# Kernel tuning notes

Hardware: AMD Instinct MI355X
Metric: run time of the kernel (lower is better)

## Reference

```python
import jax, jax.numpy as jnp
import numpy as np

DIM = 2048
H = 16
DK = 128
DV = 128
KCONV = 4
EPS = 1e-6
B = 2
S = 2048
KD = H * DK  # 2048
VD = H * DV  # 2048


def setup_inputs() -> dict:
    key = jax.random.key(0)
    ks = jax.random.split(key, 16)
    sc = 0.02
    inp = {
        "x": jax.random.normal(ks[0], (B, S, DIM), dtype=jnp.float32),
        "Wq": jax.random.normal(ks[1], (KD, DIM), dtype=jnp.float32) * sc,
        "Wk": jax.random.normal(ks[2], (KD, DIM), dtype=jnp.float32) * sc,
        "Wv": jax.random.normal(ks[3], (VD, DIM), dtype=jnp.float32) * sc,
        "Wa": jax.random.normal(ks[4], (H, DIM), dtype=jnp.float32) * sc,
        "Wb": jax.random.normal(ks[5], (H, DIM), dtype=jnp.float32) * sc,
        "Wg": jax.random.normal(ks[6], (VD, DIM), dtype=jnp.float32) * sc,
        "Wo": jax.random.normal(ks[7], (DIM, VD), dtype=jnp.float32) * sc,
        "cw_q": jax.random.normal(ks[8], (KD, KCONV), dtype=jnp.float32) * 0.3,
        "cb_q": jnp.zeros((KD,), dtype=jnp.float32),
        "cw_k": jax.random.normal(ks[9], (KD, KCONV), dtype=jnp.float32) * 0.3,
        "cb_k": jnp.zeros((KD,), dtype=jnp.float32),
        "cw_v": jax.random.normal(ks[10], (VD, KCONV), dtype=jnp.float32) * 0.3,
        "cb_v": jnp.zeros((VD,), dtype=jnp.float32),
        "A_log": jnp.zeros((H,), dtype=jnp.float32),
        "dt_bias": jnp.zeros((H,), dtype=jnp.float32),
        "norm_w": jnp.ones((VD,), dtype=jnp.float32),
    }
    return inp


def _causal_conv(x, w, b):
    # x: [B, S, C]; w: [C, K]; b: [C]. Depthwise causal conv (zero init state) + SiLU.
    Bb, Ss, C = x.shape
    xp = jnp.pad(x, ((0, 0), (KCONV - 1, 0), (0, 0)))
    out = b
    for j in range(KCONV):
        out = out + xp[:, j:j + Ss, :] * w[:, j]
    return jax.nn.silu(out)


def _l2norm(x):
    n = jnp.sqrt(jnp.sum(x * x, axis=-1, keepdims=True))
    return x / jnp.maximum(n, 1e-12)


def _forward(x, Wq, Wk, Wv, Wa, Wb, Wg, Wo, cw_q, cb_q, cw_k, cb_k, cw_v, cb_v,
             A_log, dt_bias, norm_w):
    Bb, Ss, _ = x.shape
    q = _causal_conv(x @ Wq.T, cw_q, cb_q)  # [B,S,KD]
    k = _causal_conv(x @ Wk.T, cw_k, cb_k)
    v = _causal_conv(x @ Wv.T, cw_v, cb_v)

    a = x @ Wa.T  # [B,S,H]
    b = x @ Wb.T
    g = jnp.exp(-jnp.exp(A_log)[None, None, :] * jax.nn.softplus(a + dt_bias[None, None, :]))
    beta = jax.nn.sigmoid(b)

    q = _l2norm(q.reshape(Bb, Ss, H, DK))
    k = _l2norm(k.reshape(Bb, Ss, H, DK))
    v = v.reshape(Bb, Ss, H, DV)

    S0 = jnp.zeros((Bb, H, DK, DV), dtype=x.dtype)

    def step(Sstate, inputs):
        q_t, k_t, v_t, g_t, beta_t = inputs  # [B,H,DK],[B,H,DK],[B,H,DV],[B,H],[B,H]
        retrieved = jnp.einsum('bhkv,bhk->bhv', Sstate, k_t)
        error = v_t - g_t[..., None] * retrieved
        update = k_t[..., :, None] * (beta_t[..., None] * error)[..., None, :]
        Snew = g_t[..., None, None] * Sstate + update
        o_t = jnp.einsum('bhkv,bhk->bhv', Snew, q_t)
        return Snew, o_t

    # scan over time: move time axis to front
    xs = (q.transpose(1, 0, 2, 3), k.transpose(1, 0, 2, 3), v.transpose(1, 0, 2, 3),
          g.transpose(1, 0, 2), beta.transpose(1, 0, 2))
    _, o = jax.lax.scan(step, S0, xs)  # o: [S,B,H,DV]
    o = o.transpose(1, 0, 2, 3).reshape(Bb, Ss, VD)

    # RMSNorm
    o = o * jax.lax.rsqrt(jnp.mean(o * o, axis=-1, keepdims=True) + EPS) * norm_w
    o = o * jax.nn.silu(x @ Wg.T)
    return o @ Wo.T


def reference(x, Wq, Wk, Wv, Wa, Wb, Wg, Wo, cw_q, cb_q, cw_k, cb_k, cw_v, cb_v,
              A_log, dt_bias, norm_w):
    return _forward(x, Wq, Wk, Wv, Wa, Wb, Wg, Wo, cw_q, cb_q, cw_k, cb_k,
                    cw_v, cb_v, A_log, dt_bias, norm_w)
```

## Files before the change

### kernel.cpp

```cpp
#include <hip/hip_runtime.h>

#define S_LEN   2048
#define NH      16
#define DIM     2048
#define KD      2048
#define VD      2048
#define MB      1048576ull
#define CT      64
#define NC      32

typedef short  short8  __attribute__((ext_vector_type(8)));
typedef short  short4v __attribute__((ext_vector_type(4)));
typedef float  floatx4 __attribute__((ext_vector_type(4)));

#define MFMA(a, b, c) __builtin_amdgcn_mfma_f32_16x16x32_bf16((a), (b), (c), 0, 0, 0)

__device__ inline short f2bf(float x) {
    unsigned u = __float_as_uint(x);
    unsigned r = (u + 0x7fffu + ((u >> 16) & 1u)) >> 16;
    return (short)r;
}
__device__ inline float bf2f(short s) {
    return __uint_as_float(((unsigned)(unsigned short)s) << 16);
}
__device__ inline float silu_f(float x) { return x / (1.f + __expf(-x)); }

__device__ inline short8 neg8(short8 a) {
    unsigned* p = (unsigned*)&a;
    p[0] ^= 0x80008000u; p[1] ^= 0x80008000u;
    p[2] ^= 0x80008000u; p[3] ^= 0x80008000u;
    return a;
}

__device__ inline void load_lds16(const void* g, void* l) {
    __builtin_amdgcn_global_load_lds(
        (const __attribute__((address_space(1))) unsigned int*)g,
        (__attribute__((address_space(3))) unsigned int*)l, 16, 0, 0);
}

__device__ inline void store_c(float* C, size_t idx, float v) { C[idx] = v; }
__device__ inline void store_c(short* C, size_t idx, float v) { C[idx] = f2bf(v); }

__device__ __forceinline__ void lds_barrier() {
    asm volatile("s_waitcnt lgkmcnt(0)" ::: "memory");
    __builtin_amdgcn_s_barrier();
}

__global__ __launch_bounds__(256) void cvt_all_kernel(
    const float* __restrict__ x,  const float* __restrict__ Wq,
    const float* __restrict__ Wk, const float* __restrict__ Wv,
    const float* __restrict__ Wg, const float* __restrict__ Wo,
    short* __restrict__ xb,  short* __restrict__ Wqb, short* __restrict__ Wkb,
    short* __restrict__ Wvb, short* __restrict__ Wgb, short* __restrict__ Wob) {
    const float* in; short* out; int n8;
    switch (blockIdx.y) {
        case 0:  in = x;  out = xb;  n8 = 1048576; break;
        case 1:  in = Wq; out = Wqb; n8 = 524288;  break;
        case 2:  in = Wk; out = Wkb; n8 = 524288;  break;
        case 3:  in = Wv; out = Wvb; n8 = 524288;  break;
        case 4:  in = Wg; out = Wgb; n8 = 524288;  break;
        default: in = Wo; out = Wob; n8 = 524288;  break;
    }
    int i = blockIdx.x * 256 + threadIdx.x;
    if (i >= n8) return;
    float4 a = ((const float4*)in)[2 * i];
    float4 b = ((const float4*)in)[2 * i + 1];
    short8 o;
    o[0] = f2bf(a.x); o[1] = f2bf(a.y); o[2] = f2bf(a.z); o[3] = f2bf(a.w);
    o[4] = f2bf(b.x); o[5] = f2bf(b.y); o[6] = f2bf(b.z); o[7] = f2bf(b.w);
    ((short8*)out)[i] = o;
}


#define VM(n_) asm volatile("s_waitcnt vmcnt(" #n_ ")" ::: "memory");

#define STAGE8(s_, isB_)                                                     \
    {                                                                        \
        const char* gsrc = (isB_) ? (const char*)Bw : (const char*)A;        \
        int t0 = (isB_) ? n0 : m0;                                           \
        char* dbase = smem + ((s_) & 3) * 32768 + (isB_) * 16384;            \
        _Pragma("unroll")                                                    \
        for (int ld = 0; ld < 2; ++ld) {                                     \
            int ch = ld * 8 + wave;                                          \
            int Pl = (ch << 10) + (lane << 4);                               \
            int Q  = Pl ^ (((lane >> 3) & 3) << 4);                          \
            const char* src = gsrc + ((size_t)(t0 + (Q >> 6)) << 12)         \
                              + ((size_t)(s_) << 6) + (Q & 63);              \
            load_lds16(src, dbase + (ch << 10));                             \
        }                                                                    \
    }

#define PHASE8(s_, qm_, LOADB_, STG, WAIT)                                   \
    {                                                                        \
        const char* sb = smem + ((s_) & 3) * 32768;                          \
        short8 af[4];                                                        \
        if (LOADB_) {                                                        \
            _Pragma("unroll")                                                \
            for (int nf = 0; nf < 4; ++nf)                                   \
                bfr[nf] = *(const short8*)(sb + 16384 +                      \
                    ((rowB_base + nf * 16) << 6) + qsw);                     \
        }                                                                    \
        _Pragma("unroll")                                                    \
        for (int mf = 0; mf < 4; ++mf)                                       \
            af[mf] = *(const short8*)(sb +                                   \
                ((rowA_base + (qm_) * 64 + mf * 16) << 6) + qsw);            \
        STG                                                                  \
        __builtin_amdgcn_s_barrier();                                        \
        asm volatile("s_waitcnt lgkmcnt(0)" ::: "memory");                   \
        __builtin_amdgcn_s_setprio(1);                                       \
        _Pragma("unroll")                                                    \
        for (int mf = 0; mf < 4; ++mf)                                       \
            _Pragma("unroll")                                                \
            for (int nf = 0; nf < 4; ++nf)                                   \
                acc[(qm_) * 4 + mf][nf] =                                    \
                    MFMA(af[mf], bfr[nf], acc[(qm_) * 4 + mf][nf]);          \
        __builtin_amdgcn_s_setprio(0);                                       \
        WAIT                                                                 \
        __builtin_amdgcn_s_barrier();                                        \
    }

template <typename OutT>
__device__ __forceinline__ void gemm8_tile(const short* __restrict__ A,
                                           const short* __restrict__ Bw,
                                           OutT* __restrict__ C, char* smem) {
    int x  = blockIdx.x;
    int xs = (x & 7) * 16 + (x >> 3);
    int m0 = (xs >> 3) * 256;
    int n0 = (xs & 7) * 256;
    int tid  = threadIdx.x;
    int wave = tid >> 6, lane = tid & 63;
    int l16  = lane & 15, quad = lane >> 4;
    int wm = wave >> 2, wn = wave & 3;
    int qsw = ((quad ^ ((l16 >> 1) & 3)) << 4);
    int rowA_base = wm * 128 + l16;
    int rowB_base = wn * 64 + l16;

    floatx4 acc[8][4];
#pragma unroll
    for (int i = 0; i < 8; ++i)
#pragma unroll
        for (int j = 0; j < 4; ++j) acc[i][j] = (floatx4){0.f, 0.f, 0.f, 0.f};
    short8 bfr[4];

    STAGE8(0, 0) STAGE8(0, 1)
    STAGE8(1, 0) STAGE8(1, 1)
    STAGE8(2, 0) STAGE8(2, 1)
    VM(8)
    __builtin_amdgcn_s_barrier();

#pragma unroll 1
    for (int T = 0; T < 30; ++T) {
        int s0 = 2 * T, s1 = 2 * T + 1, sa = 2 * T + 3, sb2 = 2 * T + 4;
        PHASE8(s0, 0, 1, STAGE8(sa, 0), )
        PHASE8(s0, 1, 0, STAGE8(sa, 1), VM(8))
        PHASE8(s1, 0, 1, STAGE8(sb2, 0), )
        PHASE8(s1, 1, 0, STAGE8(sb2, 1), VM(8))
    }
    PHASE8(60, 0, 1, STAGE8(63, 0), )
    PHASE8(60, 1, 0, STAGE8(63, 1), VM(8))
    PHASE8(61, 0, 1, , )
    PHASE8(61, 1, 0, , VM(4))
    PHASE8(62, 0, 1, , )
    PHASE8(62, 1, 0, , VM(0))
    PHASE8(63, 0, 1, , )
    PHASE8(63, 1, 0, , )

#pragma unroll
    for (int i = 0; i < 8; ++i) {
        int row0 = m0 + wm * 128 + (i >> 2) * 64 + (i & 3) * 16 + quad * 4;
#pragma unroll
        for (int nf = 0; nf < 4; ++nf) {
            int col = n0 + wn * 64 + nf * 16 + l16;
#pragma unroll
            for (int r = 0; r < 4; ++r)
                store_c(C, (size_t)(row0 + r) * 2048 + col, acc[i][nf][r]);
        }
    }
}

__global__ __launch_bounds__(512) void gemm8_qkvg(const short* __restrict__ A,
    const short* __restrict__ B0, const short* __restrict__ B1,
    const short* __restrict__ B2, const short* __restrict__ B3,
    short* __restrict__ C0, short* __restrict__ C1,
    short* __restrict__ C2, short* __restrict__ C3) {
    extern __shared__ char smem[];
    const short* Bw; short* C;
    switch (blockIdx.z) {
        case 0:  Bw = B0; C = C0; break;
        case 1:  Bw = B1; C = C1; break;
        case 2:  Bw = B2; C = C2; break;
        default: Bw = B3; C = C3; break;
    }
    gemm8_tile<short>(A, Bw, C, smem);
}

__global__ __launch_bounds__(512) void gemm8_out(const short* __restrict__ A,
    const short* __restrict__ Bw, float* __restrict__ C) {
    extern __shared__ char smem[];
    gemm8_tile<float>(A, Bw, C, smem);
}

__global__ __launch_bounds__(256) void ab_kernel(const float* __restrict__ x,
    const float* __restrict__ Wa, const float* __restrict__ Wb,
    const float* __restrict__ Alog, const float* __restrict__ dtb,
    float* __restrict__ gdec, float* __restrict__ beta) {
    __shared__ float xs[2048];
    __shared__ float red[32][9];
    int m = blockIdx.x, t = threadIdx.x;
    const float* xr = x + (size_t)m * DIM;
    for (int i = t; i < 512; i += 256) ((float4*)xs)[i] = ((const float4*)xr)[i];
    __syncthreads();
    int col = t >> 3, part = t & 7;
    const float* wr = (col < 16) ? (Wa + (size_t)col * DIM) : (Wb + (size_t)(col - 16) * DIM);
    float s = 0.f;
    int kb = part * 256;
#pragma unroll 4
    for (int k = 0; k < 256; k += 4) {
        float4 xv = *(const float4*)(xs + kb + k);
        float4 wv = *(const float4*)(wr + kb + k);
        s += xv.x * wv.x + xv.y * wv.y + xv.z * wv.z + xv.w * wv.w;
    }
    red[col][part] = s;
    __syncthreads();
    if (t < 32) {
        float a = 0.f;
#pragma unroll
        for (int p = 0; p < 8; ++p) a += red[t][p];
        if (t < 16) {
            float sp = a + dtb[t];
            float softp = (sp > 20.f) ? sp : log1pf(expf(sp));
            gdec[(size_t)m * NH + t] = expf(-expf(Alog[t]) * softp);
        } else {
            int h = t - 16;
            beta[(size_t)m * NH + h] = 1.f / (1.f + expf(-a));
        }
    }
}

__global__ __launch_bounds__(256) void conv_kernel(
    const short* __restrict__ qr, const short* __restrict__ kr, const short* __restrict__ vr,
    const float* __restrict__ cwq, const float* __restrict__ cbq,
    const float* __restrict__ cwk, const float* __restrict__ cbk,
    const float* __restrict__ cwv, const float* __restrict__ cbv,
    short* __restrict__ qn, short* __restrict__ kn, short* __restrict__ vc) {
    int gw   = blockIdx.x * 4 + (threadIdx.x >> 6);
    int lane = threadIdx.x & 63;
    int h  = gw & (NH - 1);
    int m  = gw >> 4;
    int tt = m & (S_LEN - 1);
    int c  = h * 128 + lane * 2;
    size_t rowbase = (size_t)m * KD + c;

    float4 wq0 = ((const float4*)cwq)[c], wq1 = ((const float4*)cwq)[c + 1];
    float4 wk0 = ((const float4*)cwk)[c], wk1 = ((const float4*)cwk)[c + 1];
    float4 wv0 = ((const float4*)cwv)[c], wv1 = ((const float4*)cwv)[c + 1];
    float q0 = cbq[c], q1 = cbq[c + 1];
    float k0 = cbk[c], k1 = cbk[c + 1];
    float v0 = cbv[c], v1 = cbv[c + 1];
    const float* wq0a = (const float*)&wq0; const float* wq1a = (const float*)&wq1;
    const float* wk0a = (const float*)&wk0; const float* wk1a = (const float*)&wk1;
    const float* wv0a = (const float*)&wv0; const float* wv1a = (const float*)&wv1;
#pragma unroll
    for (int j = 0; j < 4; ++j) {
        int ts = tt - 3 + j;
        if (ts >= 0) {
            long long rb = (long long)rowbase + (long long)(j - 3) * KD;
            unsigned uq = *(const unsigned*)(qr + rb);
            unsigned uk = *(const unsigned*)(kr + rb);
            unsigned uv = *(const unsigned*)(vr + rb);
            q0 += bf2f((short)(uq & 0xffff)) * wq0a[j]; q1 += bf2f((short)(uq >> 16)) * wq1a[j];
            k0 += bf2f((short)(uk & 0xffff)) * wk0a[j]; k1 += bf2f((short)(uk >> 16)) * wk1a[j];
            v0 += bf2f((short)(uv & 0xffff)) * wv0a[j]; v1 += bf2f((short)(uv >> 16)) * wv1a[j];
        }
    }
    q0 = silu_f(q0); q1 = silu_f(q1);
    k0 = silu_f(k0); k1 = silu_f(k1);
    v0 = silu_f(v0); v1 = silu_f(v1);

    float sq = q0 * q0 + q1 * q1;
    float sk = k0 * k0 + k1 * k1;
#pragma unroll
    for (int off = 1; off < 64; off <<= 1) {
        sq += __shfl_xor(sq, off);
        sk += __shfl_xor(sk, off);
    }
    float iq = 1.f / fmaxf(sqrtf(sq), 1e-12f);
    float ik = 1.f / fmaxf(sqrtf(sk), 1e-12f);
    unsigned oq = (unsigned)(unsigned short)f2bf(q0 * iq) | ((unsigned)(unsigned short)f2bf(q1 * iq) << 16);
    unsigned ok = (unsigned)(unsigned short)f2bf(k0 * ik) | ((unsigned)(unsigned short)f2bf(k1 * ik) << 16);
    unsigned ov = (unsigned)(unsigned short)f2bf(v0)      | ((unsigned)(unsigned short)f2bf(v1)      << 16);
    *(unsigned*)(qn + rowbase) = oq;
    *(unsigned*)(kn + rowbase) = ok;
    *(unsigned*)(vc + rowbase) = ov;
}

__global__ __launch_bounds__(256) void solve_kernel(
    const short* __restrict__ kn, const short* __restrict__ vn,
    const float* __restrict__ gdec, const float* __restrict__ beta,
    short* __restrict__ UvT, short* __restrict__ Tk) {
    __shared__ short Pn[64][72];
    __shared__ short Pt[64][72];
    __shared__ short UT[128][72];
    __shared__ float Ls[64];
    __shared__ float Bs[64];

    int wg   = blockIdx.x;
    int half = wg & 1;
    int c    = (wg >> 1) & 31;
    int bh   = wg >> 6;
    int b = bh >> 4, h = bh & 15;
    int tid = threadIdx.x;
    int wave = tid >> 6, lane = tid & 63;
    int quad = lane >> 4, l16 = lane & 15;

    const short* Kb = kn + ((size_t)(b * S_LEN + c * CT)) * KD + h * 128;
    const short* Vb = vn + ((size_t)(b * S_LEN + c * CT)) * KD + h * 128;

    if (wave == 0) {
        float lg = __logf(gdec[((size_t)(b * S_LEN + c * CT) + lane) * NH + h]);
#pragma unroll
        for (int off = 1; off < 64; off <<= 1) {
            float y = __shfl_up(lg, off);
            if (lane >= off) lg += y;
        }
        Ls[lane] = lg;
        Bs[lane] = beta[((size_t)(b * S_LEN + c * CT) + lane) * NH + h];
    }
    __syncthreads();

    {
        floatx4 acc[4];
#pragma unroll
        for (int i = 0; i < 4; ++i) acc[i] = (floatx4){0.f, 0.f, 0.f, 0.f};
        for (int ks = 0; ks < 4; ++ks) {
            short8 af = *(const short8*)(Kb + (size_t)(wave * 16 + l16) * KD + ks * 32 + quad * 8);
#pragma unroll
            for (int it = 0; it < 4; ++it) {
                short8 bf = *(const short8*)(Kb + (size_t)(it * 16 + l16) * KD + ks * 32 + quad * 8);
                acc[it] = MFMA(af, bf, acc[it]);
            }
        }
#pragma unroll
        for (int it = 0; it < 4; ++it) {
            int icol = it * 16 + l16;
#pragma unroll
            for (int r = 0; r < 4; ++r) {
                int trow = wave * 16 + quad * 4 + r;
                float v = 0.f;
                if (icol < trow) v = -Bs[trow] * __expf(Ls[trow] - Ls[icol]) * acc[it][r];
                short bv = f2bf(v);
                Pn[trow][icol] = bv;
                Pt[icol][trow] = bv;
            }
        }
    }

    {
        const short* src = half ? Kb : Vb;
        int tr = tid >> 2, seg = (tid & 3) * 32;
        float s = Bs[tr] * (half ? __expf(Ls[tr]) : 1.f);
#pragma unroll
        for (int j = 0; j < 4; ++j) {
            short8 d = *(const short8*)(src + (size_t)tr * KD + seg + j * 8);
#pragma unroll
            for (int e = 0; e < 8; ++e)
                UT[seg + j * 8 + e][tr] = f2bf(bf2f(d[e]) * s);
        }
    }
    __syncthreads();

    for (int iter = 0; iter < 6; ++iter) {
        floatx4 acc[8];
#pragma unroll
        for (int nt = 0; nt < 8; ++nt) {
            short4v u4 = *(const short4v*)&UT[nt * 16 + l16][wave * 16 + quad * 4];
            floatx4 a;
#pragma unroll
            for (int e = 0; e < 4; ++e) a[e] = bf2f(u4[e]);
            acc[nt] = a;
        }
        for (int ks = 0; ks < 2; ++ks) {
            short8 af = *(const short8*)&Pn[wave * 16 + l16][ks * 32 + quad * 8];
#pragma unroll
            for (int nt = 0; nt < 8; ++nt) {
                short8 bf = *(const short8*)&UT[nt * 16 + l16][ks * 32 + quad * 8];
                acc[nt] = MFMA(af, bf, acc[nt]);
            }
        }
        __syncthreads();
        if (iter < 5) {
#pragma unroll
            for (int nt = 0; nt < 8; ++nt) {
                short4v w4;
#pragma unroll
                for (int e = 0; e < 4; ++e) w4[e] = f2bf(acc[nt][e]);
                *(short4v*)&UT[nt * 16 + l16][wave * 16 + quad * 4] = w4;
            }
            floatx4 pacc[4];
#pragma unroll
            for (int it = 0; it < 4; ++it) pacc[it] = (floatx4){0.f, 0.f, 0.f, 0.f};
            for (int ks = 0; ks < 2; ++ks) {
                short8 paf = *(const short8*)&Pn[wave * 16 + l16][ks * 32 + quad * 8];
#pragma unroll
                for (int it = 0; it < 4; ++it) {
                    short8 pbf = *(const short8*)&Pt[it * 16 + l16][ks * 32 + quad * 8];
                    pacc[it] = MFMA(paf, pbf, pacc[it]);
                }
            }
            __syncthreads();
#pragma unroll
            for (int it = 0; it < 4; ++it) {
                int icol = it * 16 + l16;
#pragma unroll
                for (int r = 0; r < 4; ++r) {
                    int trow = wave * 16 + quad * 4 + r;
                    short bv = f2bf(pacc[it][r]);
                    Pn[trow][icol] = bv;
                    Pt[icol][trow] = bv;
                }
            }
            __syncthreads();
        } else {
            size_t cb = (size_t)(bh * NC + c);
            if (half == 0) {
#pragma unroll
                for (int nt = 0; nt < 8; ++nt) {
                    short4v w4;
#pragma unroll
                    for (int e = 0; e < 4; ++e) w4[e] = f2bf(acc[nt][e]);
                    *(short4v*)(UvT + (cb * 128 + nt * 16 + l16) * 64 + wave * 16 + quad * 4) = w4;
                }
            } else {
#pragma unroll
                for (int nt = 0; nt < 8; ++nt)
#pragma unroll
                    for (int r = 0; r < 4; ++r)
                        Tk[(cb * 64 + wave * 16 + quad * 4 + r) * 128 + nt * 16 + l16] = f2bf(acc[nt][r]);
            }
        }
    }
}

__global__ __launch_bounds__(256) void prepb_kernel(
    const short* __restrict__ qn, const short* __restrict__ kn,
    const float* __restrict__ gdec,
    short* __restrict__ Wb_, short* __restrict__ Qg,
    short* __restrict__ KtT, float* __restrict__ gam63) {
    __shared__ short KT[128][72];
    __shared__ float Ls[64];
    int wg = blockIdx.x;
    int c = wg & 31, bh = wg >> 5;
    int b = bh >> 4, h = bh & 15;
    int tid = threadIdx.x, wave = tid >> 6, lane = tid & 63;
    int quad = lane >> 4, l16 = lane & 15;
    const short* Qb = qn + ((size_t)(b * S_LEN + c * CT)) * KD + h * 128;
    const short* Kb = kn + ((size_t)(b * S_LEN + c * CT)) * KD + h * 128;

    if (wave == 0) {
        float lg = __logf(gdec[((size_t)(b * S_LEN + c * CT) + lane) * NH + h]);
#pragma unroll
        for (int off = 1; off < 64; off <<= 1) {
            float y = __shfl_up(lg, off);
            if (lane >= off) lg += y;
        }
        Ls[lane] = lg;
    }
    __syncthreads();
    size_t cb = (size_t)(bh * NC + c);
    if (tid == 0) gam63[cb] = __expf(Ls[63]);

    {
        floatx4 acc[4];
#pragma unroll
        for (int i = 0; i < 4; ++i) acc[i] = (floatx4){0.f, 0.f, 0.f, 0.f};
        for (int ks = 0; ks < 4; ++ks) {
            short8 af = *(const short8*)(Qb + (size_t)(wave * 16 + l16) * KD + ks * 32 + quad * 8);
#pragma unroll
            for (int it = 0; it < 4; ++it) {
                short8 bf = *(const short8*)(Kb + (size_t)(it * 16 + l16) * KD + ks * 32 + quad * 8);
                acc[it] = MFMA(af, bf, acc[it]);
            }
        }
#pragma unroll
        for (int it = 0; it < 4; ++it) {
            int icol = it * 16 + l16;
#pragma unroll
            for (int r = 0; r < 4; ++r) {
                int trow = wave * 16 + quad * 4 + r;
                float v = (icol <= trow) ? __expf(Ls[trow] - Ls[icol]) * acc[it][r] : 0.f;
                Wb_[(cb * 64 + trow) * 64 + icol] = f2bf(v);
            }
        }
    }

    {
        int tr = tid >> 2, seg = (tid & 3) * 32;
        float sq = __expf(Ls[tr]);
        float sk = __expf(Ls[63] - Ls[tr]);
#pragma unroll
        for (int j = 0; j < 4; ++j) {
            short8 dq = *(const short8*)(Qb + (size_t)tr * KD + seg + j * 8);
            short8 dk = *(const short8*)(Kb + (size_t)tr * KD + seg + j * 8);
            short8 oq;
#pragma unroll
            for (int e = 0; e < 8; ++e) {
                oq[e] = f2bf(bf2f(dq[e]) * sq);
                KT[seg + j * 8 + e][tr] = f2bf(bf2f(dk[e]) * sk);
            }
            *(short8*)(Qg + (cb * 64 + tr) * 128 + seg + j * 8) = oq;
        }
    }
    __syncthreads();
    {
        int dk = tid >> 1, seg = (tid & 1) * 32;
#pragma unroll
        for (int j = 0; j < 4; ++j) {
            short8 v = *(const short8*)&KT[dk][seg + j * 8];
            *(short8*)(KtT + (cb * 128 + dk) * 64 + seg + j * 8) = v;
        }
    }
}

__global__ __launch_bounds__(256, 1) void seq_kernel(
    const short* __restrict__ UvT, const short* __restrict__ Tk,
    const short* __restrict__ Wb_, const short* __restrict__ Qg,
    const short* __restrict__ KtT, const float* __restrict__ gam63,
    short* __restrict__ ob) {
    __shared__ short ST[64][136];
    __shared__ short UTs[64][72];
    int wg = blockIdx.x;
    int vh = wg & 1, bh = wg >> 1;
    int b = bh >> 4, h = bh & 15;
    int tid = threadIdx.x, wave = tid >> 6, lane = tid & 63;
    int quad = lane >> 4, l16 = lane & 15;

    for (int i = tid; i < 64 * 136; i += 256) ((short*)ST)[i] = 0;
    floatx4 sacc[8];
#pragma unroll
    for (int i = 0; i < 8; ++i) sacc[i] = (floatx4){0.f, 0.f, 0.f, 0.f};
    __syncthreads();

    short8 tkA[4], qgA[4], wA[2], ktA[16]; short4v uvA[4]; float gamA;
    short8 tkB[4], qgB[4], wB[2], ktB[16]; short4v uvB[4]; float gamB;

#define LOADF(tkX, qgX, wX, ktX, uvX, gamX, c)                                              \
    {                                                                                       \
        size_t cb = (size_t)(bh * NC + (c));                                                \
        const short* Tkc = Tk  + cb * 64 * 128;                                             \
        const short* Qgc = Qg  + cb * 64 * 128;                                             \
        const short* Wc  = Wb_ + cb * 64 * 64;                                              \
        const short* Ktc = KtT + cb * 128 * 64;                                             \
        const short* Uvc = UvT + (cb * 128 + (size_t)vh * 64) * 64;                         \
        _Pragma("unroll")                                                                   \
        for (int ks = 0; ks < 4; ++ks) {                                                    \
            tkX[ks] = *(const short8*)(Tkc + (size_t)(wave * 16 + l16) * 128 + ks * 32 + quad * 8); \
            qgX[ks] = *(const short8*)(Qgc + (size_t)(wave * 16 + l16) * 128 + ks * 32 + quad * 8); \
        }                                                                                   \
        _Pragma("unroll")                                                                   \
        for (int ks = 0; ks < 2; ++ks)                                                      \
            wX[ks] = *(const short8*)(Wc + (size_t)(wave * 16 + l16) * 64 + ks * 32 + quad * 8); \
        _Pragma("unroll")                                                                   \
        for (int dt = 0; dt < 8; ++dt)                                                      \
            _Pragma("unroll")                                                               \
            for (int ks = 0; ks < 2; ++ks)                                                  \
                ktX[dt * 2 + ks] = *(const short8*)(Ktc + (size_t)(dt * 16 + l16) * 64 + ks * 32 + quad * 8); \
        _Pragma("unroll")                                                                   \
        for (int vt = 0; vt < 4; ++vt)                                                      \
            uvX[vt] = *(const short4v*)(Uvc + (size_t)(vt * 16 + l16) * 64 + wave * 16 + quad * 4); \
        gamX = gam63[cb];                                                                   \
    }

#define BODY(tkX, qgX, wX, ktX, uvX, gamX, c)                                               \
    {                                                                                       \
        floatx4 uacc[4], oacc[4];                                                           \
        _Pragma("unroll")                                                                   \
        for (int vt = 0; vt < 4; ++vt) {                                                    \
            floatx4 a;                                                                      \
            _Pragma("unroll")                                                               \
            for (int e = 0; e < 4; ++e) a[e] = bf2f(uvX[vt][e]);                            \
            uacc[vt] = a;                                                                   \
            oacc[vt] = (floatx4){0.f, 0.f, 0.f, 0.f};                                       \
        }                                                                                   \
        _Pragma("unroll")                                                                   \
        for (int ks = 0; ks < 4; ++ks) {                                                    \
            short8 afT = neg8(tkX[ks]);                                                     \
            _Pragma("unroll")                                                               \
            for (int vt = 0; vt < 4; ++vt) {                                                \
                short8 bf = *(const short8*)&ST[vt * 16 + l16][ks * 32 + quad * 8];         \
                uacc[vt] = MFMA(afT, bf, uacc[vt]);                                         \
                oacc[vt] = MFMA(qgX[ks], bf, oacc[vt]);                                     \
            }                                                                               \
        }                                                                                   \
        _Pragma("unroll")                                                                   \
        for (int vt = 0; vt < 4; ++vt) {                                                    \
            short4v w4;                                                                     \
            _Pragma("unroll")                                                               \
            for (int e = 0; e < 4; ++e) w4[e] = f2bf(uacc[vt][e]);                          \
            *(short4v*)&UTs[vt * 16 + l16][wave * 16 + quad * 4] = w4;                      \
        }                                                                                   \
        lds_barrier();                                                                      \
        _Pragma("unroll")                                                                   \
        for (int ks = 0; ks < 2; ++ks) {                                                    \
            _Pragma("unroll")                                                               \
            for (int vt = 0; vt < 4; ++vt) {                                                \
                short8 bf = *(const short8*)&UTs[vt * 16 + l16][ks * 32 + quad * 8];        \
                oacc[vt] = MFMA(wX[ks], bf, oacc[vt]);                                      \
            }                                                                               \
        }                                                                                   \
        _Pragma("unroll")                                                                   \
        for (int vt = 0; vt < 4; ++vt)                                                      \
            _Pragma("unroll")                                                               \
            for (int r = 0; r < 4; ++r) {                                                   \
                int m = b * S_LEN + (c) * CT + wave * 16 + quad * 4 + r;                    \
                ob[(size_t)m * VD + h * 128 + vh * 64 + vt * 16 + l16] = f2bf(oacc[vt][r]); \
            }                                                                               \
        _Pragma("unroll")                                                                   \
        for (int dt = 0; dt < 8; ++dt)                                                      \
            _Pragma("unroll")                                                               \
            for (int e = 0; e < 4; ++e) sacc[dt][e] *= gamX;                                \
        _Pragma("unroll")                                                                   \
        for (int ks = 0; ks < 2; ++ks) {                                                    \
            short8 af = *(const short8*)&UTs[wave * 16 + l16][ks * 32 + quad * 8];          \
            _Pragma("unroll")                                                               \
            for (int dt = 0; dt < 8; ++dt)                                                  \
                sacc[dt] = MFMA(af, ktX[dt * 2 + ks], sacc[dt]);                            \
        }                                                                                   \
        _Pragma("unroll")                                                                   \
        for (int dt = 0; dt < 8; ++dt)                                                      \
            _Pragma("unroll")                                                               \
            for (int r = 0; r < 4; ++r)                                                     \
                ST[wave * 16 + quad * 4 + r][dt * 16 + l16] = f2bf(sacc[dt][r]);            \
        lds_barrier();                                                                      \
    }

    LOADF(tkA, qgA, wA, ktA, uvA, gamA, 0)
    for (int c = 0; c < NC; c += 2) {
        LOADF(tkB, qgB, wB, ktB, uvB, gamB, c + 1)
        BODY(tkA, qgA, wA, ktA, uvA, gamA, c)
        if (c + 2 < NC) LOADF(tkA, qgA, wA, ktA, uvA, gamA, c + 2)
        BODY(tkB, qgB, wB, ktB, uvB, gamB, c + 1)
    }
#undef LOADF
#undef BODY
}

__global__ __launch_bounds__(256) void rms_gate_kernel(
    const short* __restrict__ o, const short* __restrict__ graw,
    const float* __restrict__ nw, short* __restrict__ og) {
    __shared__ float red[4];
    int m = blockIdx.x, t = threadIdx.x;
    short8 a = ((const short8*)(o + (size_t)m * VD))[t];
    float av[8];
#pragma unroll
    for (int i = 0; i < 8; ++i) av[i] = bf2f(a[i]);
    float ss = 0.f;
#pragma unroll
    for (int i = 0; i < 8; ++i) ss += av[i] * av[i];
#pragma unroll
    for (int off = 1; off < 64; off <<= 1) ss += __shfl_xor(ss, off);
    if ((t & 63) == 0) red[t >> 6] = ss;
    __syncthreads();
    float tot = red[0] + red[1] + red[2] + red[3];
    float sc = rsqrtf(tot * (1.f / VD) + 1e-6f);
    short8 gv = ((const short8*)(graw + (size_t)m * VD))[t];
    float4 n0 = ((const float4*)nw)[2 * t];
    float4 n1 = ((const float4*)nw)[2 * t + 1];
    const float* na = (const float*)&n0;
    const float* nb = (const float*)&n1;
    short8 ov;
#pragma unroll
    for (int i = 0; i < 4; ++i) ov[i]     = f2bf(av[i]     * sc * na[i] * silu_f(bf2f(gv[i])));
#pragma unroll
    for (int i = 0; i < 4; ++i) ov[i + 4] = f2bf(av[i + 4] * sc * nb[i] * silu_f(bf2f(gv[i + 4])));
    ((short8*)(og + (size_t)m * VD))[t] = ov;
}

extern "C" void kernel_launch(void* const* d_in, const int* in_sizes, int n_in,
                              void* d_out, int out_size, void* d_ws, size_t ws_size,
                              hipStream_t stream) {
    const float* x    = (const float*)d_in[0];
    const float* Wq   = (const float*)d_in[1];
    const float* Wk   = (const float*)d_in[2];
    const float* Wv   = (const float*)d_in[3];
    const float* Wa   = (const float*)d_in[4];
    const float* Wb   = (const float*)d_in[5];
    const float* Wg   = (const float*)d_in[6];
    const float* Wo   = (const float*)d_in[7];
    const float* cwq  = (const float*)d_in[8];
    const float* cbq  = (const float*)d_in[9];
    const float* cwk  = (const float*)d_in[10];
    const float* cbk  = (const float*)d_in[11];
    const float* cwv  = (const float*)d_in[12];
    const float* cbv  = (const float*)d_in[13];
    const float* Alog = (const float*)d_in[14];
    const float* dtb  = (const float*)d_in[15];
    const float* nw   = (const float*)d_in[16];

    char* ws = (char*)d_ws;
    short* Wob = (short*)(ws);
    short* xb  = (short*)(ws + 8 * MB);
    short* Wqb = (short*)(ws + 24 * MB);
    short* Wkb = (short*)(ws + 32 * MB);
    short* Wvb = (short*)(ws + 40 * MB);
    short* Wgb = (short*)(ws + 48 * MB);
    short* qrb = (short*)(ws + 56 * MB);
    short* krb = (short*)(ws + 72 * MB);
    short* vrb = (short*)(ws + 88 * MB);
    short* grb = (short*)(ws + 104 * MB);
    short* qnb = (short*)(ws + 8 * MB);
    short* knb = (short*)(ws + 24 * MB);
    short* vnb = (short*)(ws + 40 * MB);
    float* gdec = (float*)(ws + 120 * MB);
    float* beta = (float*)(ws + 120 * MB + 262144);
    short* ob  = qrb;
    short* ogb = krb;
    short* UvT  = (short*)(ws + 121 * MB);
    short* Tkb  = (short*)(ws + 137 * MB);
    short* Wbuf = (short*)(ws + 153 * MB);
    short* Qgb  = (short*)(ws + 161 * MB);
    short* KtT  = (short*)(ws + 177 * MB);
    float* gm63 = (float*)(ws + 193 * MB);

    static bool attr_done = false;
    if (!attr_done) {
        hipFuncSetAttribute((const void*)gemm8_qkvg,
                            hipFuncAttributeMaxDynamicSharedMemorySize, 131072);
        hipFuncSetAttribute((const void*)gemm8_out,
                            hipFuncAttributeMaxDynamicSharedMemorySize, 131072);
        attr_done = true;
    }

    cvt_all_kernel<<<dim3(4096, 6), 256, 0, stream>>>(x, Wq, Wk, Wv, Wg, Wo,
                                                      xb, Wqb, Wkb, Wvb, Wgb, Wob);

    ab_kernel<<<4096, 256, 0, stream>>>(x, Wa, Wb, Alog, dtb, gdec, beta);

    gemm8_qkvg<<<dim3(128, 1, 4), 512, 131072, stream>>>(xb, Wqb, Wkb, Wvb, Wgb,
                                                         qrb, krb, vrb, grb);

    conv_kernel<<<16384, 256, 0, stream>>>(qrb, krb, vrb,
                                           cwq, cbq, cwk, cbk, cwv, cbv, qnb, knb, vnb);

    solve_kernel<<<2048, 256, 0, stream>>>(knb, vnb, gdec, beta, UvT, Tkb);
    prepb_kernel<<<1024, 256, 0, stream>>>(qnb, knb, gdec, Wbuf, Qgb, KtT, gm63);
    seq_kernel<<<64, 256, 0, stream>>>(UvT, Tkb, Wbuf, Qgb, KtT, gm63, ob);

    rms_gate_kernel<<<4096, 256, 0, stream>>>(ob, grb, nw, ogb);

    gemm8_out<<<dim3(128, 1, 1), 512, 131072, stream>>>(ogb, Wob, (float*)d_out);
}
```

Before: 745.5 us.

## Stage seq_kernel chunk operands into double-buffered LDS via async global-to-LDS loads

The sequential chunk recurrence kernel stops loading each chunk's Tk, Qg, KtT, UvT and W operands into registers. It now prefetches the next chunk into one of two LDS buffers with global_load_lds while computing the current chunk. The producer kernels write these tensors with an XOR-swizzled column layout so that the direct copies land in LDS without bank conflicts. This targets register pressure and exposed global-load latency in a kernel that runs on only 64 workgroups, at the cost of about 154KB of dynamic LDS and a hand-tuned vmcnt wait.

```diff
diff --git a/kernel.cpp b/kernel.cpp
--- a/kernel.cpp
+++ b/kernel.cpp
@@ -45,6 +45,8 @@
     asm volatile("s_waitcnt lgkmcnt(0)" ::: "memory");
     __builtin_amdgcn_s_barrier();
 }
+
+#define VM(n_) asm volatile("s_waitcnt vmcnt(" #n_ ")" ::: "memory");
 
 __global__ __launch_bounds__(256) void cvt_all_kernel(
     const float* __restrict__ x,  const float* __restrict__ Wq,
@@ -71,8 +73,6 @@
     ((short8*)out)[i] = o;
 }
 
-
-#define VM(n_) asm volatile("s_waitcnt vmcnt(" #n_ ")" ::: "memory");
 
 #define STAGE8(s_, isB_)                                                     \
     {                                                                        \
@@ -423,19 +423,23 @@
         } else {
             size_t cb = (size_t)(bh * NC + c);
             if (half == 0) {
+                int usw = (((wave * 2 + (quad >> 1)) ^ (l16 & 7)) << 3) + ((quad & 1) << 2);
 #pragma unroll
                 for (int nt = 0; nt < 8; ++nt) {
                     short4v w4;
 #pragma unroll
                     for (int e = 0; e < 4; ++e) w4[e] = f2bf(acc[nt][e]);
-                    *(short4v*)(UvT + (cb * 128 + nt * 16 + l16) * 64 + wave * 16 + quad * 4) = w4;
+                    *(short4v*)(UvT + (cb * 128 + nt * 16 + l16) * 64 + usw) = w4;
                 }
             } else {
 #pragma unroll
                 for (int nt = 0; nt < 8; ++nt)
 #pragma unroll
-                    for (int r = 0; r < 4; ++r)
-                        Tk[(cb * 64 + wave * 16 + quad * 4 + r) * 128 + nt * 16 + l16] = f2bf(acc[nt][r]);
+                    for (int r = 0; r < 4; ++r) {
+                        int trow = wave * 16 + quad * 4 + r;
+                        int colsw = (((nt * 2 + (l16 >> 3)) ^ (trow & 7)) << 3) + (l16 & 7);
+                        Tk[(cb * 64 + trow) * 128 + colsw] = f2bf(acc[nt][r]);
+                    }
             }
         }
     }
@@ -488,7 +492,8 @@
             for (int r = 0; r < 4; ++r) {
                 int trow = wave * 16 + quad * 4 + r;
                 float v = (icol <= trow) ? __expf(Ls[trow] - Ls[icol]) * acc[it][r] : 0.f;
-                Wb_[(cb * 64 + trow) * 64 + icol] = f2bf(v);
+                int colsw = (((it * 2 + (l16 >> 3)) ^ (trow & 7)) << 3) + (l16 & 7);
+                Wb_[(cb * 64 + trow) * 64 + colsw] = f2bf(v);
             }
         }
     }
@@ -507,7 +512,8 @@
                 oq[e] = f2bf(bf2f(dq[e]) * sq);
                 KT[seg + j * 8 + e][tr] = f2bf(bf2f(dk[e]) * sk);
             }
-            *(short8*)(Qg + (cb * 64 + tr) * 128 + seg + j * 8) = oq;
+            int ch = (tid & 3) * 4 + j;
+            *(short8*)(Qg + (cb * 64 + tr) * 128 + ((ch ^ (tr & 7)) << 3)) = oq;
         }
     }
     __syncthreads();
@@ -516,7 +522,8 @@
 #pragma unroll
         for (int j = 0; j < 4; ++j) {
             short8 v = *(const short8*)&KT[dk][seg + j * 8];
-            *(short8*)(KtT + (cb * 128 + dk) * 64 + seg + j * 8) = v;
+            int ch = (tid & 1) * 4 + j;
+            *(short8*)(KtT + (cb * 128 + dk) * 64 + ((ch ^ (dk & 7)) << 3)) = v;
         }
     }
 }
@@ -526,122 +533,139 @@
     const short* __restrict__ Wb_, const short* __restrict__ Qg,
     const short* __restrict__ KtT, const float* __restrict__ gam63,
     short* __restrict__ ob) {
-    __shared__ short ST[64][136];
-    __shared__ short UTs[64][72];
+    extern __shared__ char smem[];
+    const int BUF = 65536;
+    const int TKO = 0, QGO = 16384, KTO = 32768, UVO = 49152, WO = 57344;
+    short (*ST)[136] = (short (*)[136])(smem + 131072);
+    short (*UTs)[72] = (short (*)[72])(smem + 131072 + 17408);
+
     int wg = blockIdx.x;
     int vh = wg & 1, bh = wg >> 1;
     int b = bh >> 4, h = bh & 15;
     int tid = threadIdx.x, wave = tid >> 6, lane = tid & 63;
     int quad = lane >> 4, l16 = lane & 15;
-
-    for (int i = tid; i < 64 * 136; i += 256) ((short*)ST)[i] = 0;
+    int swk = l16 & 7;
+
+    for (int i = tid; i < 64 * 136; i += 256) ((short*)(smem + 131072))[i] = 0;
     floatx4 sacc[8];
 #pragma unroll
     for (int i = 0; i < 8; ++i) sacc[i] = (floatx4){0.f, 0.f, 0.f, 0.f};
+
+    size_t cb0 = (size_t)bh * NC;
+    int row16 = wave * 16 + l16;
+    int chq[4];
+#pragma unroll
+    for (int ks = 0; ks < 4; ++ks) chq[ks] = (((ks * 4 + quad) ^ swk) << 4);
+    int uvoff = (((wave * 2 + (quad >> 1)) ^ swk) << 4) + ((quad & 1) << 3);
+
+#define STAGE_CHUNK(bsel_, c_)                                                       \
+    {                                                                                \
+        char* dst = smem + (bsel_) * BUF;                                            \
+        size_t cbs = cb0 + (c_);                                                     \
+        const char* gt = (const char*)Tk  + cbs * 16384 + wave * 1024 + lane * 16;   \
+        const char* gq = (const char*)Qg  + cbs * 16384 + wave * 1024 + lane * 16;   \
+        const char* gk = (const char*)KtT + cbs * 16384 + wave * 1024 + lane * 16;   \
+        const char* gu = (const char*)UvT + cbs * 16384 + (size_t)vh * 8192 + wave * 1024 + lane * 16; \
+        const char* gw = (const char*)Wb_ + cbs * 8192  + wave * 1024 + lane * 16;   \
+        _Pragma("unroll")                                                            \
+        for (int it = 0; it < 4; ++it) {                                             \
+            load_lds16(gt + it * 4096, dst + TKO + it * 4096 + wave * 1024);         \
+            load_lds16(gq + it * 4096, dst + QGO + it * 4096 + wave * 1024);         \
+            load_lds16(gk + it * 4096, dst + KTO + it * 4096 + wave * 1024);         \
+        }                                                                            \
+        _Pragma("unroll")                                                            \
+        for (int it = 0; it < 2; ++it) {                                             \
+            load_lds16(gu + it * 4096, dst + UVO + it * 4096 + wave * 1024);         \
+            load_lds16(gw + it * 4096, dst + WO  + it * 4096 + wave * 1024);         \
+        }                                                                            \
+    }
+
+    STAGE_CHUNK(0, 0)
+    float gamA = gam63[cb0];
     __syncthreads();
 
-    short8 tkA[4], qgA[4], wA[2], ktA[16]; short4v uvA[4]; float gamA;
-    short8 tkB[4], qgB[4], wB[2], ktB[16]; short4v uvB[4]; float gamB;
-
-#define LOADF(tkX, qgX, wX, ktX, uvX, gamX, c)                                              \
-    {                                                                                       \
-        size_t cb = (size_t)(bh * NC + (c));                                                \
-        const short* Tkc = Tk  + cb * 64 * 128;                                             \
-        const short* Qgc = Qg  + cb * 64 * 128;                                             \
-        const short* Wc  = Wb_ + cb * 64 * 64;                                              \
-        const short* Ktc = KtT + cb * 128 * 64;                                             \
-        const short* Uvc = UvT + (cb * 128 + (size_t)vh * 64) * 64;                         \
-        _Pragma("unroll")                                                                   \
-        for (int ks = 0; ks < 4; ++ks) {                                                    \
-            tkX[ks] = *(const short8*)(Tkc + (size_t)(wave * 16 + l16) * 128 + ks * 32 + quad * 8); \
-            qgX[ks] = *(const short8*)(Qgc + (size_t)(wave * 16 + l16) * 128 + ks * 32 + quad * 8); \
-        }                                                                                   \
-        _Pragma("unroll")                                                                   \
-        for (int ks = 0; ks < 2; ++ks)                                                      \
-            wX[ks] = *(const short8*)(Wc + (size_t)(wave * 16 + l16) * 64 + ks * 32 + quad * 8); \
-        _Pragma("unroll")                                                                   \
-        for (int dt = 0; dt < 8; ++dt)                                                      \
-            _Pragma("unroll")                                                               \
-            for (int ks = 0; ks < 2; ++ks)                                                  \
-                ktX[dt * 2 + ks] = *(const short8*)(Ktc + (size_t)(dt * 16 + l16) * 64 + ks * 32 + quad * 8); \
-        _Pragma("unroll")                                                                   \
-        for (int vt = 0; vt < 4; ++vt)                                                      \
-            uvX[vt] = *(const short4v*)(Uvc + (size_t)(vt * 16 + l16) * 64 + wave * 16 + quad * 4); \
-        gamX = gam63[cb];                                                                   \
-    }
-
-#define BODY(tkX, qgX, wX, ktX, uvX, gamX, c)                                               \
-    {                                                                                       \
-        floatx4 uacc[4], oacc[4];                                                           \
-        _Pragma("unroll")                                                                   \
-        for (int vt = 0; vt < 4; ++vt) {                                                    \
-            floatx4 a;                                                                      \
-            _Pragma("unroll")                                                               \
-            for (int e = 0; e < 4; ++e) a[e] = bf2f(uvX[vt][e]);                            \
-            uacc[vt] = a;                                                                   \
-            oacc[vt] = (floatx4){0.f, 0.f, 0.f, 0.f};                                       \
-        }                                                                                   \
-        _Pragma("unroll")                                                                   \
-        for (int ks = 0; ks < 4; ++ks) {                                                    \
-            short8 afT = neg8(tkX[ks]);                                                     \
-            _Pragma("unroll")                                                               \
-            for (int vt = 0; vt < 4; ++vt) {                                                \
-                short8 bf = *(const short8*)&ST[vt * 16 + l16][ks * 32 + quad * 8];         \
-                uacc[vt] = MFMA(afT, bf, uacc[vt]);                                         \
-                oacc[vt] = MFMA(qgX[ks], bf, oacc[vt]);                                     \
-            }                                                                               \
-        }                                                                                   \
-        _Pragma("unroll")                                                                   \
-        for (int vt = 0; vt < 4; ++vt) {                                                    \
-            short4v w4;                                                                     \
-            _Pragma("unroll")                                                               \
-            for (int e = 0; e < 4; ++e) w4[e] = f2bf(uacc[vt][e]);                          \
-            *(short4v*)&UTs[vt * 16 + l16][wave * 16 + quad * 4] = w4;                      \
-        }                                                                                   \
-        lds_barrier();                                                                      \
-        _Pragma("unroll")                                                                   \
-        for (int ks = 0; ks < 2; ++ks) {                                                    \
-            _Pragma("unroll")                                                               \
-            for (int vt = 0; vt < 4; ++vt) {                                                \
-                short8 bf = *(const short8*)&UTs[vt * 16 + l16][ks * 32 + quad * 8];        \
-                oacc[vt] = MFMA(wX[ks], bf, oacc[vt]);                                      \
-            }                                                                               \
-        }                                                                                   \
-        _Pragma("unroll")                                                                   \
-        for (int vt = 0; vt < 4; ++vt)                                                      \
-            _Pragma("unroll")                                                               \
-            for (int r = 0; r < 4; ++r) {                                                   \
-                int m = b * S_LEN + (c) * CT + wave * 16 + quad * 4 + r;                    \
-                ob[(size_t)m * VD + h * 128 + vh * 64 + vt * 16 + l16] = f2bf(oacc[vt][r]); \
-            }                                                                               \
-        _Pragma("unroll")                                                                   \
-        for (int dt = 0; dt < 8; ++dt)                                                      \
-            _Pragma("unroll")                                                               \
-            for (int e = 0; e < 4; ++e) sacc[dt][e] *= gamX;                                \
-        _Pragma("unroll")                                                                   \
-        for (int ks = 0; ks < 2; ++ks) {                                                    \
-            short8 af = *(const short8*)&UTs[wave * 16 + l16][ks * 32 + quad * 8];          \
-            _Pragma("unroll")                                                               \
-            for (int dt = 0; dt < 8; ++dt)                                                  \
-                sacc[dt] = MFMA(af, ktX[dt * 2 + ks], sacc[dt]);                            \
-        }                                                                                   \
-        _Pragma("unroll")                                                                   \
-        for (int dt = 0; dt < 8; ++dt)                                                      \
-            _Pragma("unroll")                                                               \
-            for (int r = 0; r < 4; ++r)                                                     \
-                ST[wave * 16 + quad * 4 + r][dt * 16 + l16] = f2bf(sacc[dt][r]);            \
-        lds_barrier();                                                                      \
-    }
-
-    LOADF(tkA, qgA, wA, ktA, uvA, gamA, 0)
-    for (int c = 0; c < NC; c += 2) {
-        LOADF(tkB, qgB, wB, ktB, uvB, gamB, c + 1)
-        BODY(tkA, qgA, wA, ktA, uvA, gamA, c)
-        if (c + 2 < NC) LOADF(tkA, qgA, wA, ktA, uvA, gamA, c + 2)
-        BODY(tkB, qgB, wB, ktB, uvB, gamB, c + 1)
-    }
-#undef LOADF
-#undef BODY
+#pragma unroll 1
+    for (int c = 0; c < NC; ++c) {
+        float gamN = 0.f;
+        if (c + 1 < NC) {
+            gamN = gam63[cb0 + c + 1];
+            STAGE_CHUNK((c + 1) & 1, c + 1)
+        }
+        const char* bufc = smem + (c & 1) * BUF;
+
+        floatx4 uacc[4], oacc[4];
+#pragma unroll
+        for (int vt = 0; vt < 4; ++vt) {
+            short4v u4 = *(const short4v*)(bufc + UVO + (vt * 16 + l16) * 128 + uvoff);
+            floatx4 a;
+#pragma unroll
+            for (int e = 0; e < 4; ++e) a[e] = bf2f(u4[e]);
+            uacc[vt] = a;
+            oacc[vt] = (floatx4){0.f, 0.f, 0.f, 0.f};
+        }
+#pragma unroll
+        for (int ks = 0; ks < 4; ++ks) {
+            short8 tkf = *(const short8*)(bufc + TKO + row16 * 256 + chq[ks]);
+            short8 qgf = *(const short8*)(bufc + QGO + row16 * 256 + chq[ks]);
+            short8 afT = neg8(tkf);
+#pragma unroll
+            for (int vt = 0; vt < 4; ++vt) {
+                short8 bf = *(const short8*)&ST[vt * 16 + l16][ks * 32 + quad * 8];
+                uacc[vt] = MFMA(afT, bf, uacc[vt]);
+                oacc[vt] = MFMA(qgf, bf, oacc[vt]);
+            }
+        }
+#pragma unroll
+        for (int vt = 0; vt < 4; ++vt) {
+            short4v w4;
+#pragma unroll
+            for (int e = 0; e < 4; ++e) w4[e] = f2bf(uacc[vt][e]);
+            *(short4v*)&UTs[vt * 16 + l16][wave * 16 + quad * 4] = w4;
+        }
+        lds_barrier();
+#pragma unroll
+        for (int ks = 0; ks < 2; ++ks) {
+            short8 wf = *(const short8*)(bufc + WO + row16 * 128 + chq[ks]);
+#pragma unroll
+            for (int vt = 0; vt < 4; ++vt) {
+                short8 bf = *(const short8*)&UTs[vt * 16 + l16][ks * 32 + quad * 8];
+                oacc[vt] = MFMA(wf, bf, oacc[vt]);
+            }
+        }
+#pragma unroll
+        for (int vt = 0; vt < 4; ++vt)
+#pragma unroll
+            for (int r = 0; r < 4; ++r) {
+                int m = b * S_LEN + c * CT + wave * 16 + quad * 4 + r;
+                ob[(size_t)m * VD + h * 128 + vh * 64 + vt * 16 + l16] = f2bf(oacc[vt][r]);
+            }
+#pragma unroll
+        for (int dt = 0; dt < 8; ++dt)
+#pragma unroll
+            for (int e = 0; e < 4; ++e) sacc[dt][e] *= gamA;
+#pragma unroll
+        for (int ks = 0; ks < 2; ++ks) {
+            short8 af = *(const short8*)&UTs[wave * 16 + l16][ks * 32 + quad * 8];
+#pragma unroll
+            for (int dt = 0; dt < 8; ++dt) {
+                short8 ktf = *(const short8*)(bufc + KTO + (dt * 16 + l16) * 128 + chq[ks]);
+                sacc[dt] = MFMA(af, ktf, sacc[dt]);
+            }
+        }
+#pragma unroll
+        for (int dt = 0; dt < 8; ++dt)
+#pragma unroll
+            for (int r = 0; r < 4; ++r)
+                ST[wave * 16 + quad * 4 + r][dt * 16 + l16] = f2bf(sacc[dt][r]);
+
+        if (c + 1 < NC) {
+            asm volatile("s_waitcnt lgkmcnt(0)" ::: "memory");
+            VM(16)
+            __builtin_amdgcn_s_barrier();
+        }
+        gamA = gamN;
+    }
+#undef STAGE_CHUNK
 }
 
 __global__ __launch_bounds__(256) void rms_gate_kernel(
@@ -727,6 +751,8 @@
                             hipFuncAttributeMaxDynamicSharedMemorySize, 131072);
         hipFuncSetAttribute((const void*)gemm8_out,
                             hipFuncAttributeMaxDynamicSharedMemorySize, 131072);
+        hipFuncSetAttribute((const void*)seq_kernel,
+                            hipFuncAttributeMaxDynamicSharedMemorySize, 157696);
         attr_done = true;
     }
 
@@ -743,7 +769,7 @@
 
     solve_kernel<<<2048, 256, 0, stream>>>(knb, vnb, gdec, beta, UvT, Tkb);
     prepb_kernel<<<1024, 256, 0, stream>>>(qnb, knb, gdec, Wbuf, Qgb, KtT, gm63);
-    seq_kernel<<<64, 256, 0, stream>>>(UvT, Tkb, Wbuf, Qgb, KtT, gm63, ob);
+    seq_kernel<<<64, 256, 157696, stream>>>(UvT, Tkb, Wbuf, Qgb, KtT, gm63, ob);
 
     rms_gate_kernel<<<4096, 256, 0, stream>>>(ob, grb, nw, ogb);
 
```

After: 723.3 us. 3.0% less time.
